# Performance work log

Hardware: AMD Instinct MI355X
Metric: run time of the kernel (lower is better)

The kernel has to match this reference:

```python
import jax, jax.numpy as jnp
import numpy as np

DIM = 256
NUM_HEADS = 4
HEAD_DIM = DIM // NUM_HEADS
WINDOW_SIZES = [2, 4, 8, 16]
SCALE = HEAD_DIM ** -0.5


def setup_inputs() -> dict:
    key = jax.random.key(0)
    k1, k2, k3, k4 = jax.random.split(key, 4)
    B, C, H, W = 8, DIM, 128, 128
    x = jax.random.normal(k1, (B, C, H, W), dtype=jnp.float32)
    # 1x1 conv weights stored as [out, in]
    qkv_w = jax.random.normal(k2, (3 * DIM, DIM), dtype=jnp.float32) * (DIM ** -0.5)
    proj_w = jax.random.normal(k3, (DIM, DIM), dtype=jnp.float32) * (DIM ** -0.5)
    proj_b = jax.random.normal(k4, (DIM,), dtype=jnp.float32) * 0.01
    return {"x": x, "qkv_w": qkv_w, "proj_w": proj_w, "proj_b": proj_b}


def _window_attn(q, k, v, ws):
    # q,k,v: [B, H, W, hd] for one head; windowed self-attention of size ws
    B, H, W, hd = q.shape
    hg, wg = H // ws, W // ws

    def part(t):
        # [B,H,W,hd] -> [B, hg*wg, ws*ws, hd]
        t = t.reshape(B, hg, ws, wg, ws, hd).transpose(0, 1, 3, 2, 4, 5)
        return t.reshape(B, hg * wg, ws * ws, hd)

    qw, kw, vw = part(q), part(k), part(v)
    attn = jnp.einsum('bgqd,bgkd->bgqk', qw, kw) * SCALE
    attn = jax.nn.softmax(attn, axis=-1)
    out = jnp.einsum('bgqk,bgkd->bgqd', attn, vw)
    # reassemble: [B, hg, wg, ws, ws, hd] -> [B, H, W, hd]
    out = out.reshape(B, hg, wg, ws, ws, hd).transpose(0, 1, 3, 2, 4, 5)
    return out.reshape(B, H, W, hd)


def reference(x, qkv_w, proj_w, proj_b):
    B, C, H, W = x.shape
    # 1x1 conv qkv: [B, 3*dim, H, W] -> [3, B, nh, H, W, hd]
    qkv = jnp.einsum('bchw,oc->bohw', x, qkv_w)
    qkv = qkv.reshape(B, 3, NUM_HEADS, HEAD_DIM, H, W).transpose(1, 0, 2, 4, 5, 3)
    q, k, v = qkv[0], qkv[1], qkv[2]
    outs = []
    for i, ws in enumerate(WINDOW_SIZES):
        outs.append(_window_attn(q[:, i], k[:, i], v[:, i], ws))
    y = jnp.concatenate(outs, axis=-1)  # [B, H, W, dim]
    y = jnp.einsum('bhwc,oc->bhwo', y, proj_w) + proj_b
    y = y.transpose(0, 3, 1, 2)  # [B, dim, H, W]
    return y + x
```

## Files before the change

kernel.cpp:

```cpp
#include <hip/hip_runtime.h>
#include <hip/hip_bf16.h>
#include <cstddef>
#include <cstdint>

typedef unsigned short u16;
typedef unsigned int uint32;
typedef __attribute__((ext_vector_type(8))) short bf16x8;
typedef __attribute__((ext_vector_type(4))) float f32x4;

#define SPATIAL 16384
#define TOTAL_M 131072

__device__ __forceinline__ u16 f2b(float f) {
  __hip_bfloat16 h = __float2bfloat16(f);
  return *reinterpret_cast<u16*>(&h);
}
__device__ __forceinline__ uint32 pk2(float a, float b) {
  return (uint32)f2b(a) | ((uint32)f2b(b) << 16);
}
__device__ __forceinline__ float blo(uint32 u) {
  union { uint32 u; float f; } c; c.u = u << 16; return c.f;
}
__device__ __forceinline__ float bhi(uint32 u) {
  union { uint32 u; float f; } c; c.u = u & 0xffff0000u; return c.f;
}

__device__ __forceinline__ void gload_lds16(const u16* g, u16* l) {
  __builtin_amdgcn_global_load_lds(
      (const __attribute__((address_space(1))) void*)g,
      (__attribute__((address_space(3))) void*)l, 16, 0, 0);
}

template <int WS>
__device__ __forceinline__ size_t tok_base(int gw, int tt) {
  constexpr int WG = 128 / WS;
  constexpr int NWIN = WG * WG;
  int bb = gw / NWIN, rr = gw % NWIN;
  int gy = rr / WG, gx = rr % WG;
  int yy = gy * WS + tt / WS, xx = gx * WS + tt % WS;
  return (((size_t)bb * 128 + yy) * 128 + xx) * 768;
}

__global__ __launch_bounds__(256) void prep(const float* __restrict__ x,
                                            const float* __restrict__ qw,
                                            const float* __restrict__ pw,
                                            u16* __restrict__ xT,
                                            u16* __restrict__ wq,
                                            u16* __restrict__ wp) {
  const int tid = threadIdx.x;
  const int bid = blockIdx.x;
  if (bid >= 2048) {
    const int t = (bid - 2048) * 256 + tid;
#pragma unroll
    for (int i = 0; i < 16; ++i) {
      const int e = i * 4096 + t;
      if (e < 49152) {
        float4 v = *(const float4*)&qw[(size_t)e * 4];
        ushort4 o;
        o.x = f2b(v.x); o.y = f2b(v.y); o.z = f2b(v.z); o.w = f2b(v.w);
        *(ushort4*)&wq[(size_t)e * 4] = o;
      } else {
        float4 v = *(const float4*)&pw[(size_t)(e - 49152) * 4];
        ushort4 o;
        o.x = f2b(v.x); o.y = f2b(v.y); o.z = f2b(v.z); o.w = f2b(v.w);
        *(ushort4*)&wp[(size_t)(e - 49152) * 4] = o;
      }
    }
    return;
  }
  __shared__ u16 Ts[64 * 256];
  const int b = bid >> 8;
  const int sp0 = (bid & 255) * 64;
#pragma unroll
  for (int it = 0; it < 16; ++it) {
    int e = it * 256 + tid;
    int k = e >> 4;
    int c4 = (e & 15) * 4;
    float4 v = *(const float4*)&x[(((size_t)(b * 256 + k)) << 14) + sp0 + c4];
    Ts[(c4 + 0) * 256 + (k ^ ((((c4 + 0)) & 31) << 3))] = f2b(v.x);
    Ts[(c4 + 1) * 256 + (k ^ ((((c4 + 1)) & 31) << 3))] = f2b(v.y);
    Ts[(c4 + 2) * 256 + (k ^ ((((c4 + 2)) & 31) << 3))] = f2b(v.z);
    Ts[(c4 + 3) * 256 + (k ^ ((((c4 + 3)) & 31) << 3))] = f2b(v.w);
  }
  __syncthreads();
#pragma unroll
  for (int it = 0; it < 8; ++it) {
    int e = it * 256 + tid;
    int sp = e >> 5;
    int kc = (e & 31) * 8;
    bf16x8 row = *(const bf16x8*)&Ts[sp * 256 + (kc ^ ((sp & 31) << 3))];
    *(bf16x8*)&xT[((size_t)(b * 16384 + sp0 + sp)) * 256 + kc] = row;
  }
}

__global__ __launch_bounds__(256) void gemm_qkv(const u16* __restrict__ xT,
                                                const u16* __restrict__ wq,
                                                u16* __restrict__ qkv) {
  __shared__ u16 As[2][128 * 64];
  __shared__ u16 Bs[2][128 * 64];
  const int tid = threadIdx.x;
  const int bid = blockIdx.x;
  const int logical = (bid & 7) * 768 + (bid >> 3);
  const int m0 = (logical / 6) * 128;
  const int n0 = (logical % 6) * 128;
  const int lane = tid & 63, w = tid >> 6;
  const int wr = w >> 1, wc = w & 1;
  const int fr = lane & 15, fk = lane >> 4;
  const int frx = (fr & 7) << 3;
  const int kcs = ((tid & 7) * 8) ^ (((tid >> 3) & 7) << 3);
  const int srow = tid >> 3;
  f32x4 acc[4][4] = {};

#define STAGE_QKV(B, KT)                                                     \
  do {                                                                       \
    const int k0s = (KT)*64;                                                 \
    _Pragma("unroll") for (int it = 0; it < 4; ++it) {                       \
      int row = it * 32 + srow;                                              \
      u16* la = &As[B][(it * 256 + (tid & 192)) * 8];                        \
      u16* lb = &Bs[B][(it * 256 + (tid & 192)) * 8];                        \
      gload_lds16(&xT[((size_t)(m0 + row) << 8) + k0s + kcs], la);           \
      gload_lds16(&wq[((size_t)(n0 + row) << 8) + k0s + kcs], lb);           \
    }                                                                        \
  } while (0)

#define COMP_QKV(B)                                                          \
  do {                                                                       \
    _Pragma("unroll") for (int kk = 0; kk < 2; ++kk) {                       \
      const int kb = (kk * 32 + fk * 8) ^ frx;                               \
      bf16x8 af[4], bfr[4];                                                  \
      _Pragma("unroll") for (int i = 0; i < 4; ++i) {                        \
        af[i] = *(const bf16x8*)&As[B][(wr * 64 + i * 16 + fr) * 64 + kb];   \
        bfr[i] = *(const bf16x8*)&Bs[B][(wc * 64 + i * 16 + fr) * 64 + kb];  \
      }                                                                      \
      _Pragma("unroll") for (int i = 0; i < 4; ++i)                          \
          _Pragma("unroll") for (int j = 0; j < 4; ++j) acc[i][j] =          \
          __builtin_amdgcn_mfma_f32_16x16x32_bf16(bfr[j], af[i],             \
                                                  acc[i][j], 0, 0, 0);       \
    }                                                                        \
  } while (0)

#define PHASE(WAITN)                                                         \
  asm volatile("s_waitcnt vmcnt(" #WAITN ")" ::: "memory");                  \
  __builtin_amdgcn_s_barrier();                                              \
  __builtin_amdgcn_sched_barrier(0)

#define PHASE_END()                                                          \
  __builtin_amdgcn_sched_barrier(0);                                         \
  __builtin_amdgcn_s_barrier()

  STAGE_QKV(0, 0);
  STAGE_QKV(1, 1);
  PHASE(8);
  COMP_QKV(0);
  PHASE_END();
  STAGE_QKV(0, 2);
  PHASE(8);
  COMP_QKV(1);
  PHASE_END();
  STAGE_QKV(1, 3);
  PHASE(8);
  COMP_QKV(0);
  PHASE_END();
  PHASE(0);
  COMP_QKV(1);
#undef STAGE_QKV
#undef COMP_QKV
#undef PHASE
#undef PHASE_END

#pragma unroll
  for (int i = 0; i < 4; ++i) {
    const size_t row = (size_t)(m0 + wr * 64 + i * 16 + fr) * 768;
#pragma unroll
    for (int j = 0; j < 4; ++j) {
      uint2 p;
      p.x = pk2(acc[i][j][0], acc[i][j][1]);
      p.y = pk2(acc[i][j][2], acc[i][j][3]);
      *(uint2*)&qkv[row + n0 + wc * 64 + j * 16 + fk * 4] = p;
    }
  }
}

template <int WS>
__device__ __forceinline__ void win_attn_body(u16* __restrict__ qkv, int head,
                                              int bid, u16 (*Ks)[68], u16 (*Vs)[68]) {
  constexpr int T = WS * WS;
  constexpr int G = 256 / T;
  const int tid = threadIdx.x;
  const int gw0 = bid * G;
  const int qoff = head * 64;

#pragma unroll
  for (int i = 0; i < 16; ++i) {
    int e4 = i * 256 + tid;
    int tok = e4 >> 4;
    int d4 = (e4 & 15) * 4;
    size_t base = tok_base<WS>(gw0 + tok / T, tok % T);
    *(uint2*)&Ks[tok][d4] = *(const uint2*)&qkv[base + 256 + qoff + d4];
    *(uint2*)&Vs[tok][d4] = *(const uint2*)&qkv[base + 512 + qoff + d4];
  }
  __syncthreads();

  const int myw = tid / T;
  const int mytt = tid % T;
  const size_t mybase = tok_base<WS>(gw0 + myw, mytt);

  float q[64];
#pragma unroll
  for (int d4 = 0; d4 < 16; ++d4) {
    uint2 q2 = *(const uint2*)&qkv[mybase + qoff + d4 * 4];
    q[d4 * 4 + 0] = blo(q2.x); q[d4 * 4 + 1] = bhi(q2.x);
    q[d4 * 4 + 2] = blo(q2.y); q[d4 * 4 + 3] = bhi(q2.y);
  }
  const int rbase = myw * T;

  float mmax = -1e30f, lsum = 0.f;
  for (int j = 0; j < T; ++j) {
    float s = 0.f;
#pragma unroll
    for (int d4 = 0; d4 < 16; ++d4) {
      uint2 k2 = *(const uint2*)&Ks[rbase + j][d4 * 4];
      s = fmaf(q[d4 * 4 + 0], blo(k2.x), s);
      s = fmaf(q[d4 * 4 + 1], bhi(k2.x), s);
      s = fmaf(q[d4 * 4 + 2], blo(k2.y), s);
      s = fmaf(q[d4 * 4 + 3], bhi(k2.y), s);
    }
    s *= 0.125f;
    const float mn = fmaxf(mmax, s);
    lsum = lsum * __expf(mmax - mn) + __expf(s - mn);
    mmax = mn;
  }
  const float inv = 1.f / lsum;

  float acc[64] = {};
  for (int j = 0; j < T; ++j) {
    float s = 0.f;
#pragma unroll
    for (int d4 = 0; d4 < 16; ++d4) {
      uint2 k2 = *(const uint2*)&Ks[rbase + j][d4 * 4];
      s = fmaf(q[d4 * 4 + 0], blo(k2.x), s);
      s = fmaf(q[d4 * 4 + 1], bhi(k2.x), s);
      s = fmaf(q[d4 * 4 + 2], blo(k2.y), s);
      s = fmaf(q[d4 * 4 + 3], bhi(k2.y), s);
    }
    const float p = __expf(s * 0.125f - mmax) * inv;
#pragma unroll
    for (int d4 = 0; d4 < 16; ++d4) {
      uint2 v2 = *(const uint2*)&Vs[rbase + j][d4 * 4];
      acc[d4 * 4 + 0] = fmaf(p, blo(v2.x), acc[d4 * 4 + 0]);
      acc[d4 * 4 + 1] = fmaf(p, bhi(v2.x), acc[d4 * 4 + 1]);
      acc[d4 * 4 + 2] = fmaf(p, blo(v2.y), acc[d4 * 4 + 2]);
      acc[d4 * 4 + 3] = fmaf(p, bhi(v2.y), acc[d4 * 4 + 3]);
    }
  }
#pragma unroll
  for (int d4 = 0; d4 < 16; ++d4) {
    uint2 o2;
    o2.x = pk2(acc[d4 * 4 + 0], acc[d4 * 4 + 1]);
    o2.y = pk2(acc[d4 * 4 + 2], acc[d4 * 4 + 3]);
    *(uint2*)&qkv[mybase + qoff + d4 * 4] = o2;
  }
}

__global__ __launch_bounds__(256) void win_small(u16* __restrict__ qkv) {
  __shared__ u16 Ks[256][68];
  __shared__ u16 Vs[256][68];
  if (blockIdx.x < 512)
    win_attn_body<2>(qkv, 0, blockIdx.x, Ks, Vs);
  else
    win_attn_body<4>(qkv, 1, blockIdx.x - 512, Ks, Vs);
}

template <int WS>
__global__ __launch_bounds__(256) void win_attn_mfma(u16* __restrict__ qkv, int head) {
  constexpr int T = WS * WS;
  constexpr int G = 256 / T;
  constexpr int KT = T / 16;
  constexpr int KS = T / 32;
  constexpr int PL = T + 8;
  __shared__ u16 Ks[256 * 72];
  __shared__ u16 Vt[64 * 264];
  __shared__ u16 Plds[4 * 16 * PL];
  const int tid = threadIdx.x;
  const int gw0 = blockIdx.x * G;
  const int qoff = head * 64;

#pragma unroll
  for (int it = 0; it < 16; ++it) {
    int e = it * 256 + tid;
    int tok = e >> 4;
    int d4 = (e & 15) * 4;
    int win = tok / T, tt = tok % T;
    size_t base = tok_base<WS>(gw0 + win, tt);
    uint2 kk = *(const uint2*)&qkv[base + 256 + qoff + d4];
    uint2 vv = *(const uint2*)&qkv[base + 512 + qoff + d4];
    *(uint2*)&Ks[tok * 72 + d4] = kk;
    Vt[(d4 + 0) * 264 + tok] = (u16)(vv.x & 0xffffu);
    Vt[(d4 + 1) * 264 + tok] = (u16)(vv.x >> 16);
    Vt[(d4 + 2) * 264 + tok] = (u16)(vv.y & 0xffffu);
    Vt[(d4 + 3) * 264 + tok] = (u16)(vv.y >> 16);
  }
  __syncthreads();

  const int w = tid >> 6, lane = tid & 63;
  const int fr = lane & 15, fk = lane >> 4;
  u16* prow = &Plds[(w * 16 + fr) * PL];

  for (int qi = 0; qi < 4; ++qi) {
    const int qg = w * 4 + qi;
    const int win = qg / (T / 16);
    const int qt = qg % (T / 16);
    const int gw = gw0 + win;

    const size_t qb = tok_base<WS>(gw, qt * 16 + fr) + qoff;
    bf16x8 qf[2];
#pragma unroll
    for (int ds = 0; ds < 2; ++ds)
      qf[ds] = *(const bf16x8*)&qkv[qb + ds * 32 + fk * 8];

    f32x4 sv[KT];
#pragma unroll
    for (int kt = 0; kt < KT; ++kt) {
      const u16* krow = &Ks[(win * T + kt * 16 + fr) * 72];
      bf16x8 k0 = *(const bf16x8*)&krow[fk * 8];
      bf16x8 k1 = *(const bf16x8*)&krow[32 + fk * 8];
      f32x4 s = {};
      s = __builtin_amdgcn_mfma_f32_16x16x32_bf16(k0, qf[0], s, 0, 0, 0);
      s = __builtin_amdgcn_mfma_f32_16x16x32_bf16(k1, qf[1], s, 0, 0, 0);
      sv[kt] = s;
    }

    float rmax = -3e38f;
#pragma unroll
    for (int kt = 0; kt < KT; ++kt)
#pragma unroll
      for (int r = 0; r < 4; ++r) rmax = fmaxf(rmax, sv[kt][r]);
    rmax = fmaxf(rmax, __shfl_xor(rmax, 16));
    rmax = fmaxf(rmax, __shfl_xor(rmax, 32));
    const float m = rmax * 0.125f;
    float l = 0.f;
#pragma unroll
    for (int kt = 0; kt < KT; ++kt)
#pragma unroll
      for (int r = 0; r < 4; ++r) {
        float ev = __expf(sv[kt][r] * 0.125f - m);
        sv[kt][r] = ev;
        l += ev;
      }
    l += __shfl_xor(l, 16);
    l += __shfl_xor(l, 32);
    const float linv = 1.f / l;

#pragma unroll
    for (int kt = 0; kt < KT; ++kt) {
      uint2 pp;
      pp.x = pk2(sv[kt][0], sv[kt][1]);
      pp.y = pk2(sv[kt][2], sv[kt][3]);
      *(uint2*)&prow[kt * 16 + fk * 4] = pp;
    }
    __asm__ __volatile__("s_waitcnt lgkmcnt(0)" ::: "memory");
    __builtin_amdgcn_sched_barrier(0);

    f32x4 ov[4] = {};
#pragma unroll
    for (int ks = 0; ks < KS; ++ks) {
      bf16x8 pf = *(const bf16x8*)&prow[ks * 32 + fk * 8];
#pragma unroll
      for (int dt = 0; dt < 4; ++dt) {
        bf16x8 vf = *(const bf16x8*)&Vt[(dt * 16 + fr) * 264 + win * T + ks * 32 + fk * 8];
        ov[dt] = __builtin_amdgcn_mfma_f32_16x16x32_bf16(pf, vf, ov[dt], 0, 0, 0);
      }
    }

#pragma unroll
    for (int r = 0; r < 4; ++r) {
      float lr = __shfl(linv, fk * 4 + r);
      size_t ob = tok_base<WS>(gw, qt * 16 + fk * 4 + r) + qoff;
#pragma unroll
      for (int dt = 0; dt < 4; ++dt)
        qkv[ob + dt * 16 + fr] = f2b(ov[dt][r] * lr);
    }
  }
}

__global__ __launch_bounds__(256) void gemm_proj(const u16* __restrict__ qkv,
                                                 const u16* __restrict__ wp,
                                                 const float* __restrict__ bias,
                                                 const float* __restrict__ x,
                                                 float* __restrict__ out) {
  __shared__ u16 As[2][128 * 64];
  __shared__ u16 Bs[2][128 * 64];
  const int tid = threadIdx.x;
  const int bid = blockIdx.x;
  const int logical = (bid & 7) * 256 + (bid >> 3);
  const int m0 = (logical >> 1) * 128;
  const int n0 = (logical & 1) * 128;
  const int lane = tid & 63, w = tid >> 6;
  const int wr = w >> 1, wc = w & 1;
  const int fr = lane & 15, fk = lane >> 4;
  const int frx = (fr & 7) << 3;
  const int kcs = ((tid & 7) * 8) ^ (((tid >> 3) & 7) << 3);
  const int srow = tid >> 3;
  const int b = m0 >> 14;
  f32x4 acc[4][4] = {};

#define STAGE_PRJ(B, KT)                                                     \
  do {                                                                       \
    const int k0s = (KT)*64;                                                 \
    _Pragma("unroll") for (int it = 0; it < 4; ++it) {                       \
      int row = it * 32 + srow;                                              \
      u16* la = &As[B][(it * 256 + (tid & 192)) * 8];                        \
      u16* lb = &Bs[B][(it * 256 + (tid & 192)) * 8];                        \
      gload_lds16(&qkv[(size_t)(m0 + row) * 768 + k0s + kcs], la);           \
      gload_lds16(&wp[((size_t)(n0 + row) << 8) + k0s + kcs], lb);           \
    }                                                                        \
  } while (0)

#define COMP_PRJ(B)                                                          \
  do {                                                                       \
    _Pragma("unroll") for (int kk = 0; kk < 2; ++kk) {                       \
      const int kb = (kk * 32 + fk * 8) ^ frx;                               \
      bf16x8 af[4], bfr[4];                                                  \
      _Pragma("unroll") for (int i = 0; i < 4; ++i) {                        \
        af[i] = *(const bf16x8*)&As[B][(wr * 64 + i * 16 + fr) * 64 + kb];   \
        bfr[i] = *(const bf16x8*)&Bs[B][(wc * 64 + i * 16 + fr) * 64 + kb];  \
      }                                                                      \
      _Pragma("unroll") for (int i = 0; i < 4; ++i)                          \
          _Pragma("unroll") for (int j = 0; j < 4; ++j) acc[i][j] =          \
          __builtin_amdgcn_mfma_f32_16x16x32_bf16(af[i], bfr[j],             \
                                                  acc[i][j], 0, 0, 0);       \
    }                                                                        \
  } while (0)

#define PHASE(WAITN)                                                         \
  asm volatile("s_waitcnt vmcnt(" #WAITN ")" ::: "memory");                  \
  __builtin_amdgcn_s_barrier();                                              \
  __builtin_amdgcn_sched_barrier(0)

#define PHASE_END()                                                          \
  __builtin_amdgcn_sched_barrier(0);                                         \
  __builtin_amdgcn_s_barrier()

  STAGE_PRJ(0, 0);
  STAGE_PRJ(1, 1);
  PHASE(8);
  COMP_PRJ(0);
  PHASE_END();
  STAGE_PRJ(0, 2);
  PHASE(8);
  COMP_PRJ(1);
  PHASE_END();
  STAGE_PRJ(1, 3);
  PHASE(8);
  COMP_PRJ(0);
  PHASE_END();
  PHASE(0);
  COMP_PRJ(1);
#undef STAGE_PRJ
#undef COMP_PRJ
#undef PHASE
#undef PHASE_END

#pragma unroll
  for (int i = 0; i < 4; ++i) {
    const int sp = (m0 & 16383) + wr * 64 + i * 16 + fk * 4;
#pragma unroll
    for (int j = 0; j < 4; ++j) {
      const int n = n0 + wc * 64 + j * 16 + fr;
      const size_t o = ((size_t)(b * 256 + n) << 14) + sp;
      const float4 r4 = *(const float4*)&x[o];
      const float bb = bias[n];
      float4 v = make_float4(acc[i][j][0] + bb + r4.x, acc[i][j][1] + bb + r4.y,
                             acc[i][j][2] + bb + r4.z, acc[i][j][3] + bb + r4.w);
      *(float4*)&out[o] = v;
    }
  }
}

extern "C" void kernel_launch(void* const* d_in, const int* in_sizes, int n_in,
                              void* d_out, int out_size, void* d_ws, size_t ws_size,
                              hipStream_t stream) {
  const float* x = (const float*)d_in[0];
  const float* qkv_w = (const float*)d_in[1];
  const float* proj_w = (const float*)d_in[2];
  const float* proj_b = (const float*)d_in[3];
  float* out = (float*)d_out;
  u16* qkv = (u16*)d_ws;
  u16* xT = qkv + (size_t)131072 * 768;
  u16* wq = xT + (size_t)131072 * 256;
  u16* wp = wq + (size_t)768 * 256;

  prep<<<2064, 256, 0, stream>>>(x, qkv_w, proj_w, xT, wq, wp);
  gemm_qkv<<<6144, 256, 0, stream>>>(xT, wq, qkv);
  win_small<<<1024, 256, 0, stream>>>(qkv);
  win_attn_mfma<8><<<512, 256, 0, stream>>>(qkv, 2);
  win_attn_mfma<16><<<512, 256, 0, stream>>>(qkv, 3);
  gemm_proj<<<2048, 256, 0, stream>>>(qkv, wp, proj_b, x, out);
}
```

Measured before the change: 334.6 us.

## Fuse x transpose and bf16 conversion into QKV GEMM A-tile loading

Removes the separate prep pass that transposed x into a bf16 token-major buffer. The QKV GEMM now reads fp32 x directly, converts it to bf16 and writes it transposed into a swizzled LDS tile. Weight conversion moves to a small standalone kernel. This saves one full write and read of the xT intermediate. In exchange, the GEMM drops its double-buffered async global-to-LDS pipeline for a single buffer with __syncthreads, and each of the six N-tiles re-reads and re-converts the same fp32 x data.

```diff
diff --git a/kernel.cpp b/kernel.cpp
--- a/kernel.cpp
+++ b/kernel.cpp
@@ -41,133 +41,90 @@
   return (((size_t)bb * 128 + yy) * 128 + xx) * 768;
 }
 
-__global__ __launch_bounds__(256) void prep(const float* __restrict__ x,
-                                            const float* __restrict__ qw,
-                                            const float* __restrict__ pw,
-                                            u16* __restrict__ xT,
-                                            u16* __restrict__ wq,
-                                            u16* __restrict__ wp) {
-  const int tid = threadIdx.x;
-  const int bid = blockIdx.x;
-  if (bid >= 2048) {
-    const int t = (bid - 2048) * 256 + tid;
-#pragma unroll
-    for (int i = 0; i < 16; ++i) {
-      const int e = i * 4096 + t;
-      if (e < 49152) {
-        float4 v = *(const float4*)&qw[(size_t)e * 4];
-        ushort4 o;
-        o.x = f2b(v.x); o.y = f2b(v.y); o.z = f2b(v.z); o.w = f2b(v.w);
-        *(ushort4*)&wq[(size_t)e * 4] = o;
-      } else {
-        float4 v = *(const float4*)&pw[(size_t)(e - 49152) * 4];
-        ushort4 o;
-        o.x = f2b(v.x); o.y = f2b(v.y); o.z = f2b(v.z); o.w = f2b(v.w);
-        *(ushort4*)&wp[(size_t)(e - 49152) * 4] = o;
-      }
-    }
-    return;
-  }
-  __shared__ u16 Ts[64 * 256];
-  const int b = bid >> 8;
-  const int sp0 = (bid & 255) * 64;
-#pragma unroll
-  for (int it = 0; it < 16; ++it) {
-    int e = it * 256 + tid;
-    int k = e >> 4;
-    int c4 = (e & 15) * 4;
-    float4 v = *(const float4*)&x[(((size_t)(b * 256 + k)) << 14) + sp0 + c4];
-    Ts[(c4 + 0) * 256 + (k ^ ((((c4 + 0)) & 31) << 3))] = f2b(v.x);
-    Ts[(c4 + 1) * 256 + (k ^ ((((c4 + 1)) & 31) << 3))] = f2b(v.y);
-    Ts[(c4 + 2) * 256 + (k ^ ((((c4 + 2)) & 31) << 3))] = f2b(v.z);
-    Ts[(c4 + 3) * 256 + (k ^ ((((c4 + 3)) & 31) << 3))] = f2b(v.w);
-  }
-  __syncthreads();
-#pragma unroll
-  for (int it = 0; it < 8; ++it) {
-    int e = it * 256 + tid;
-    int sp = e >> 5;
-    int kc = (e & 31) * 8;
-    bf16x8 row = *(const bf16x8*)&Ts[sp * 256 + (kc ^ ((sp & 31) << 3))];
-    *(bf16x8*)&xT[((size_t)(b * 16384 + sp0 + sp)) * 256 + kc] = row;
-  }
-}
-
-__global__ __launch_bounds__(256) void gemm_qkv(const u16* __restrict__ xT,
+__global__ __launch_bounds__(256) void wprep(const float* __restrict__ qw,
+                                             const float* __restrict__ pw,
+                                             u16* __restrict__ wq,
+                                             u16* __restrict__ wp) {
+  const int t = blockIdx.x * 256 + threadIdx.x;
+#pragma unroll
+  for (int i = 0; i < 16; ++i) {
+    const int e = i * 4096 + t;
+    if (e < 49152) {
+      float4 v = *(const float4*)&qw[(size_t)e * 4];
+      ushort4 o;
+      o.x = f2b(v.x); o.y = f2b(v.y); o.z = f2b(v.z); o.w = f2b(v.w);
+      *(ushort4*)&wq[(size_t)e * 4] = o;
+    } else {
+      float4 v = *(const float4*)&pw[(size_t)(e - 49152) * 4];
+      ushort4 o;
+      o.x = f2b(v.x); o.y = f2b(v.y); o.z = f2b(v.z); o.w = f2b(v.w);
+      *(ushort4*)&wp[(size_t)(e - 49152) * 4] = o;
+    }
+  }
+}
+
+__global__ __launch_bounds__(256) void gemm_qkv(const float* __restrict__ x,
                                                 const u16* __restrict__ wq,
                                                 u16* __restrict__ qkv) {
-  __shared__ u16 As[2][128 * 64];
-  __shared__ u16 Bs[2][128 * 64];
+  __shared__ u16 As[128 * 64];
+  __shared__ u16 Bs[128 * 64];
   const int tid = threadIdx.x;
   const int bid = blockIdx.x;
   const int logical = (bid & 7) * 768 + (bid >> 3);
   const int m0 = (logical / 6) * 128;
   const int n0 = (logical % 6) * 128;
+  const int b = m0 >> 14;
+  const int sp0 = m0 & 16383;
   const int lane = tid & 63, w = tid >> 6;
   const int wr = w >> 1, wc = w & 1;
   const int fr = lane & 15, fk = lane >> 4;
   const int frx = (fr & 7) << 3;
   const int kcs = ((tid & 7) * 8) ^ (((tid >> 3) & 7) << 3);
   const int srow = tid >> 3;
+  const int spq = tid & 31;
+  const int kq8 = tid >> 5;
   f32x4 acc[4][4] = {};
-
-#define STAGE_QKV(B, KT)                                                     \
-  do {                                                                       \
-    const int k0s = (KT)*64;                                                 \
-    _Pragma("unroll") for (int it = 0; it < 4; ++it) {                       \
-      int row = it * 32 + srow;                                              \
-      u16* la = &As[B][(it * 256 + (tid & 192)) * 8];                        \
-      u16* lb = &Bs[B][(it * 256 + (tid & 192)) * 8];                        \
-      gload_lds16(&xT[((size_t)(m0 + row) << 8) + k0s + kcs], la);           \
-      gload_lds16(&wq[((size_t)(n0 + row) << 8) + k0s + kcs], lb);           \
-    }                                                                        \
-  } while (0)
-
-#define COMP_QKV(B)                                                          \
-  do {                                                                       \
-    _Pragma("unroll") for (int kk = 0; kk < 2; ++kk) {                       \
-      const int kb = (kk * 32 + fk * 8) ^ frx;                               \
-      bf16x8 af[4], bfr[4];                                                  \
-      _Pragma("unroll") for (int i = 0; i < 4; ++i) {                        \
-        af[i] = *(const bf16x8*)&As[B][(wr * 64 + i * 16 + fr) * 64 + kb];   \
-        bfr[i] = *(const bf16x8*)&Bs[B][(wc * 64 + i * 16 + fr) * 64 + kb];  \
-      }                                                                      \
-      _Pragma("unroll") for (int i = 0; i < 4; ++i)                          \
-          _Pragma("unroll") for (int j = 0; j < 4; ++j) acc[i][j] =          \
-          __builtin_amdgcn_mfma_f32_16x16x32_bf16(bfr[j], af[i],             \
-                                                  acc[i][j], 0, 0, 0);       \
-    }                                                                        \
-  } while (0)
-
-#define PHASE(WAITN)                                                         \
-  asm volatile("s_waitcnt vmcnt(" #WAITN ")" ::: "memory");                  \
-  __builtin_amdgcn_s_barrier();                                              \
-  __builtin_amdgcn_sched_barrier(0)
-
-#define PHASE_END()                                                          \
-  __builtin_amdgcn_sched_barrier(0);                                         \
-  __builtin_amdgcn_s_barrier()
-
-  STAGE_QKV(0, 0);
-  STAGE_QKV(1, 1);
-  PHASE(8);
-  COMP_QKV(0);
-  PHASE_END();
-  STAGE_QKV(0, 2);
-  PHASE(8);
-  COMP_QKV(1);
-  PHASE_END();
-  STAGE_QKV(1, 3);
-  PHASE(8);
-  COMP_QKV(0);
-  PHASE_END();
-  PHASE(0);
-  COMP_QKV(1);
-#undef STAGE_QKV
-#undef COMP_QKV
-#undef PHASE
-#undef PHASE_END
-
+  for (int kt = 0; kt < 4; ++kt) {
+    const int k0 = kt * 64;
+#pragma unroll
+    for (int it = 0; it < 4; ++it) {
+      int row = it * 32 + srow;
+      u16* lb = &Bs[(it * 256 + (tid & 192)) * 8];
+      gload_lds16(&wq[((size_t)(n0 + row) << 8) + k0 + kcs], lb);
+    }
+    float4 xa[8];
+#pragma unroll
+    for (int j = 0; j < 8; ++j)
+      xa[j] = *(const float4*)&x[(((size_t)(b * 256 + k0 + kq8 * 8 + j)) << 14) + sp0 + spq * 4];
+#pragma unroll
+    for (int s = 0; s < 4; ++s) {
+      const int sp = spq * 4 + s;
+      union { bf16x8 v; uint32 u[4]; } U;
+      U.u[0] = pk2(((const float*)&xa[0])[s], ((const float*)&xa[1])[s]);
+      U.u[1] = pk2(((const float*)&xa[2])[s], ((const float*)&xa[3])[s]);
+      U.u[2] = pk2(((const float*)&xa[4])[s], ((const float*)&xa[5])[s]);
+      U.u[3] = pk2(((const float*)&xa[6])[s], ((const float*)&xa[7])[s]);
+      const int ch = kq8 ^ (sp & 7);
+      *(bf16x8*)&As[sp * 64 + ch * 8] = U.v;
+    }
+    __syncthreads();
+#pragma unroll
+    for (int kk = 0; kk < 2; ++kk) {
+      const int kb = (kk * 32 + fk * 8) ^ frx;
+      bf16x8 af[4], bfr[4];
+#pragma unroll
+      for (int i = 0; i < 4; ++i) {
+        af[i] = *(const bf16x8*)&As[(wr * 64 + i * 16 + fr) * 64 + kb];
+        bfr[i] = *(const bf16x8*)&Bs[(wc * 64 + i * 16 + fr) * 64 + kb];
+      }
+#pragma unroll
+      for (int i = 0; i < 4; ++i)
+#pragma unroll
+        for (int j = 0; j < 4; ++j)
+          acc[i][j] = __builtin_amdgcn_mfma_f32_16x16x32_bf16(bfr[j], af[i], acc[i][j], 0, 0, 0);
+    }
+    __syncthreads();
+  }
 #pragma unroll
   for (int i = 0; i < 4; ++i) {
     const size_t row = (size_t)(m0 + wr * 64 + i * 16 + fr) * 768;
@@ -486,12 +443,11 @@
   const float* proj_b = (const float*)d_in[3];
   float* out = (float*)d_out;
   u16* qkv = (u16*)d_ws;
-  u16* xT = qkv + (size_t)131072 * 768;
-  u16* wq = xT + (size_t)131072 * 256;
+  u16* wq = qkv + (size_t)131072 * 768;
   u16* wp = wq + (size_t)768 * 256;
 
-  prep<<<2064, 256, 0, stream>>>(x, qkv_w, proj_w, xT, wq, wp);
-  gemm_qkv<<<6144, 256, 0, stream>>>(xT, wq, qkv);
+  wprep<<<16, 256, 0, stream>>>(qkv_w, proj_w, wq, wp);
+  gemm_qkv<<<6144, 256, 0, stream>>>(x, wq, qkv);
   win_small<<<1024, 256, 0, stream>>>(qkv);
   win_attn_mfma<8><<<512, 256, 0, stream>>>(qkv, 2);
   win_attn_mfma<16><<<512, 256, 0, stream>>>(qkv, 3);
```

Result: slower. 352.2 us (+5.3%).
